# Kernel optimization log

Measured on AMD Instinct MI355X. Metric: run time of the kernel, lower is better.

The kernel has to match this reference:

```python
import jax, jax.numpy as jnp
import numpy as np

EPSILON = 0.1
N_ITERS = 5
SCALE = 0.05  # keeps exp(-cdist/epsilon) from underflowing to 0


def setup_inputs() -> dict:
    key = jax.random.key(0)
    k1, k2 = jax.random.split(key)
    P = jax.random.normal(k1, (8192, 64), dtype=jnp.float32) * SCALE
    Q = jax.random.normal(k2, (8192, 64), dtype=jnp.float32) * SCALE
    return {"P": P, "Q": Q}


def _cdist(P, Q):
    # Euclidean pairwise distances via the mm expansion (like torch.cdist p=2)
    sq = (jnp.sum(P * P, axis=-1)[:, None]
          + jnp.sum(Q * Q, axis=-1)[None, :]
          - 2.0 * P @ Q.T)
    return jnp.sqrt(jnp.maximum(sq, 0.0))


def reference(P, Q):
    C = _cdist(P, Q)                      # [N, N]
    K = jnp.exp(-C / EPSILON)             # [N, N]
    D = P.shape[1]
    u = jnp.ones((P.shape[0],), dtype=P.dtype) / D
    for _ in range(N_ITERS):              # small fixed iteration count
        v = 1.0 / (K @ u)                 # [N]
        u = 1.0 / (K @ v)                 # [N]
    plan = u[:, None] * K * v[None, :]    # [N, N]
    return jnp.sum(plan * C)
```

## Files before the change

kernel.cpp:

```cpp
#include <hip/hip_runtime.h>
#include <hip/hip_fp16.h>
#include <stdint.h>

#define NROWS 8192
#define DIM 64
#define EPS 0.1f

typedef float f32x4 __attribute__((ext_vector_type(4)));
typedef short s16x8 __attribute__((ext_vector_type(8)));
typedef _Float16 h2 __attribute__((ext_vector_type(2)));


__device__ __forceinline__ float wave_reduce_add(float v) {
  #pragma unroll
  for (int off = 32; off > 0; off >>= 1) v += __shfl_down(v, off, 64);
  return v;
}

__device__ __forceinline__ uint32_t pack_bf16_trunc(float x, float y) {
  return __builtin_amdgcn_perm(__float_as_uint(y), __float_as_uint(x), 0x07060302u);
}

__device__ __forceinline__ int pi_idx(int i) {
  int r = i & 63;
  int tj = r >> 4, quad = (r >> 2) & 3, e = r & 3;
  return (i & ~63) | (quad * 16 + tj * 4 + e);
}


#if __has_builtin(__builtin_amdgcn_cvt_scalef32_pk_f16_fp4)
#define CVT4H(kd, sel) __builtin_amdgcn_cvt_scalef32_pk_f16_fp4((kd), 1.0f, (sel))
#else
__device__ __forceinline__ h2 cvt4h_fb(uint32_t kd, int sel) {
  uint32_t byt  = (kd >> (sel * 8)) & 0xFFu;
  uint32_t selv = (byt & 0xFu) | ((byt >> 4) << 16);
  uint32_t tb = __builtin_amdgcn_perm(0x46444240u, 0x3E3C3800u, selv);
  uint32_t d  = ((tb & 0xFFu) << 8) | ((tb & 0xFF0000u) << 8);
  return __builtin_bit_cast(h2, d);
}
#define CVT4H(kd, sel) cvt4h_fb((kd), (sel))
#endif

#if __has_builtin(__builtin_amdgcn_cvt_scalef32_pk_fp4_f32)
__device__ __forceinline__ uint32_t enc4(float q0, float q1, float q2, float q3) {
  uint32_t pk = __builtin_amdgcn_cvt_scalef32_pk_fp4_f32(0u, q0, q1, 1.0f, 0);
  pk = __builtin_amdgcn_cvt_scalef32_pk_fp4_f32(pk, q2, q3, 1.0f, 1);
  return pk & 0xFFFFu;
}
#else
__device__ __forceinline__ uint32_t enc1(float q) {
  float c = fminf(floorf(2.f * q + 0.5f), 4.f);
  c += (q > 2.5f) ? 1.f : 0.f;
  c += (q > 3.5f) ? 1.f : 0.f;
  return (uint32_t)c;
}
__device__ __forceinline__ uint32_t enc4(float q0, float q1, float q2, float q3) {
  return enc1(q0) | (enc1(q1) << 4) | (enc1(q2) << 8) | (enc1(q3) << 12);
}
#endif

#if __has_builtin(__builtin_amdgcn_exp2f)
#define EXPD(d) __builtin_amdgcn_exp2f(-14.4269504089f * (d))
#else
#define EXPD(d) __expf(-10.0f * (d))
#endif

#define FP4DOT(kd, xv, acc)                                                          \
  acc = __builtin_amdgcn_fdot2(CVT4H((kd), 0), __builtin_bit_cast(h2, (xv).x), acc, false); \
  acc = __builtin_amdgcn_fdot2(CVT4H((kd), 1), __builtin_bit_cast(h2, (xv).y), acc, false); \
  acc = __builtin_amdgcn_fdot2(CVT4H((kd), 2), __builtin_bit_cast(h2, (xv).z), acc, false); \
  acc = __builtin_amdgcn_fdot2(CVT4H((kd), 3), __builtin_bit_cast(h2, (xv).w), acc, false);

#define FIN1(kd, xd_, sel)                                                           \
  {                                                                                  \
    uint32_t byt  = ((kd) >> ((sel) * 8)) & 0xFFu;                                   \
    uint32_t selv = (byt & 0xFu) | ((byt & 0xF0u) << 12);                            \
    uint32_t hi = __builtin_amdgcn_perm(0x4945423Du, 0x3800B500u, selv);             \
    uint32_t lo = __builtin_amdgcn_perm(0x608C978Cu, 0xDE008C00u, selv);             \
    h2 lut = __builtin_bit_cast(h2, lo | (hi << 8));                                 \
    h2 xp  = __builtin_bit_cast(h2, (xd_));                                          \
    s1b = __builtin_amdgcn_fdot2(CVT4H((kd), (sel)), xp, s1b, false);                \
    t2b = __builtin_amdgcn_fdot2(lut, xp, t2b, false);                               \
  }
#define FINDOT(kd, xv) FIN1(kd, (xv).x, 0) FIN1(kd, (xv).y, 1) FIN1(kd, (xv).z, 2) FIN1(kd, (xv).w, 3)


__global__ __launch_bounds__(256) void rownorm_pack(
    const float* __restrict__ P, const float* __restrict__ Q,
    float* __restrict__ p2, float* __restrict__ q2,
    unsigned short* __restrict__ Pb, unsigned short* __restrict__ Qb) {
  int g = blockIdx.x * 256 + threadIdx.x;
  int row = g >> 3, sub = g & 7;
  const float* X;
  float* out;
  unsigned short* Xb;
  int r;
  float sc;
  if (row < NROWS) { X = P; out = p2; Xb = Pb; r = row; sc = -2.f; }
  else             { X = Q; out = q2; Xb = Qb; r = row - NROWS; sc = 1.f; }
  const float4* X4 = (const float4*)(X + (size_t)r * DIM);
  float4 a0 = X4[sub * 2], a1 = X4[sub * 2 + 1];
  float ss = a0.x * a0.x + a0.y * a0.y + a0.z * a0.z + a0.w * a0.w
           + a1.x * a1.x + a1.y * a1.y + a1.z * a1.z + a1.w * a1.w;
  ss += __shfl_xor(ss, 1, 64);
  ss += __shfl_xor(ss, 2, 64);
  ss += __shfl_xor(ss, 4, 64);
  if (sub == 0) out[r] = ss;
  uint4 pk;
  pk.x = pack_bf16_trunc(sc * a0.x, sc * a0.y);
  pk.y = pack_bf16_trunc(sc * a0.z, sc * a0.w);
  pk.z = pack_bf16_trunc(sc * a1.x, sc * a1.y);
  pk.w = pack_bf16_trunc(sc * a1.z, sc * a1.w);
  *(uint4*)(Xb + (size_t)r * DIM + sub * 8) = pk;
}


struct KgenSmem {
  unsigned char A[128 * 128];
  unsigned char B[256 * 128];
};

__device__ __forceinline__ int swiz_off(int row, int kc) {
  return row * 128 + ((kc ^ (row & 7)) << 4);
}

__global__ __launch_bounds__(512) void kgen_kernel(
    const unsigned short* __restrict__ Pb, const unsigned short* __restrict__ Qb,
    const float* __restrict__ p2, const float* __restrict__ q2,
    unsigned char* __restrict__ K4, unsigned char* __restrict__ scales,
    float* __restrict__ rspart) {
  __shared__ KgenSmem sm;
  const int t  = threadIdx.x;
  const int bi = blockIdx.x * 128;
  const int bj = blockIdx.y * 256;

  {
    const uint4* Pb4 = (const uint4*)(Pb + (size_t)bi * DIM);
    const uint4* Qb4 = (const uint4*)(Qb + (size_t)bj * DIM);
    #pragma unroll
    for (int it = 0; it < 2; ++it) {
      int idx = t + it * 512;
      int row = idx >> 3, kc = idx & 7;
      *(uint4*)(sm.A + swiz_off(row, kc)) = Pb4[row * 8 + kc];
    }
    #pragma unroll
    for (int it = 0; it < 4; ++it) {
      int idx = t + it * 512;
      int row = idx >> 3, kc = idx & 7;
      *(uint4*)(sm.B + swiz_off(row, kc)) = Qb4[row * 8 + kc];
    }
  }
  __syncthreads();

  const int w        = t >> 6;
  const int lane     = t & 63;
  const int quad     = lane >> 4;
  const int m16      = lane & 15;
  const int wave_row = (w >> 2) * 64;
  const int wave_col = (w & 3) * 64;

  float pn[4];
  f32x4 qn[4];
  #pragma unroll
  for (int ti = 0; ti < 4; ++ti) pn[ti] = p2[bi + wave_row + ti * 16 + m16];
  #pragma unroll
  for (int tj = 0; tj < 4; ++tj)
    qn[tj] = *(const f32x4*)&q2[bj + wave_col + tj * 16 + quad * 4];

  f32x4 acc[4][4];
  #pragma unroll
  for (int ti = 0; ti < 4; ++ti)
    #pragma unroll
    for (int tj = 0; tj < 4; ++tj) acc[ti][tj] = qn[tj] + pn[ti];

  #pragma unroll
  for (int kstep = 0; kstep < 2; ++kstep) {
    const int kc = kstep * 4 + quad;
    s16x8 af[4], bf[4];
    #pragma unroll
    for (int ti = 0; ti < 4; ++ti)
      af[ti] = *(const s16x8*)(sm.A + swiz_off(wave_row + ti * 16 + m16, kc));
    #pragma unroll
    for (int tj = 0; tj < 4; ++tj)
      bf[tj] = *(const s16x8*)(sm.B + swiz_off(wave_col + tj * 16 + m16, kc));
    #pragma unroll
    for (int ti = 0; ti < 4; ++ti)
      #pragma unroll
      for (int tj = 0; tj < 4; ++tj)
        acc[ti][tj] = __builtin_amdgcn_mfma_f32_16x16x32_bf16(
            bf[tj], af[ti], acc[ti][tj], 0, 0, 0);
  }

  #pragma unroll
  for (int ti = 0; ti < 4; ++ti) {
    const int row = bi + wave_row + ti * 16 + m16;
    float kv[4][4];
    float mx = 0.f, rs = 0.f;
    #pragma unroll
    for (int tj = 0; tj < 4; ++tj) {
      f32x4 sq = acc[ti][tj];
      kv[tj][0] = EXPD(__builtin_amdgcn_sqrtf(fmaxf(sq.x, 0.f)));
      kv[tj][1] = EXPD(__builtin_amdgcn_sqrtf(fmaxf(sq.y, 0.f)));
      kv[tj][2] = EXPD(__builtin_amdgcn_sqrtf(fmaxf(sq.z, 0.f)));
      kv[tj][3] = EXPD(__builtin_amdgcn_sqrtf(fmaxf(sq.w, 0.f)));
      float mt = fmaxf(fmaxf(kv[tj][0], kv[tj][1]), fmaxf(kv[tj][2], kv[tj][3]));
      mx = fmaxf(mx, mt);
      rs += (kv[tj][0] + kv[tj][1]) + (kv[tj][2] + kv[tj][3]);
    }
    mx = fmaxf(mx, __shfl_xor(mx, 16, 64));
    uint32_t eb = (__float_as_uint(mx) >> 23) - 1u;
    float si = __uint_as_float((254u - eb) << 23);
    uint32_t pk0 = enc4(kv[0][0] * si, kv[0][1] * si, kv[0][2] * si, kv[0][3] * si);
    uint32_t pk1 = enc4(kv[1][0] * si, kv[1][1] * si, kv[1][2] * si, kv[1][3] * si);
    uint32_t pk2 = enc4(kv[2][0] * si, kv[2][1] * si, kv[2][2] * si, kv[2][3] * si);
    uint32_t pk3 = enc4(kv[3][0] * si, kv[3][1] * si, kv[3][2] * si, kv[3][3] * si);
    uint2 st = uint2{pk0 | (pk1 << 16), pk2 | (pk3 << 16)};
    *(uint2*)(K4 + (size_t)row * (NROWS / 2) + ((bj + wave_col) >> 1) + quad * 8) = st;
    uint32_t eb2 = (uint32_t)__shfl_xor((int)eb, 32, 64);
    if (quad == 0) {
      *(unsigned short*)(scales + (size_t)row * 256 + ((bj + wave_col) >> 5)) =
          (unsigned short)((eb & 0xFFu) | ((eb2 & 0xFFu) << 8));
    }
    float v = rs;
    v += __shfl_xor(v, 16, 64);
    v += __shfl_xor(v, 32, 64);
    if (quad == 0)
      rspart[(size_t)(blockIdx.y * 4 + (w & 3)) * NROWS + row] = v;
  }
}

__global__ __launch_bounds__(128) void v1_kernel(const float* __restrict__ rspart,
                                                 unsigned short* __restrict__ vb16) {
  int i = blockIdx.x * 128 + threadIdx.x;
  float s = 0.f;
  #pragma unroll 8
  for (int c = 0; c < 128; ++c) s += rspart[(size_t)c * NROWS + i];
  vb16[pi_idx(i)] = __half_as_ushort(__float2half(64.0f / s));
}


__global__ __launch_bounds__(256) void matvec_fp4(
    const unsigned char* __restrict__ K4, const unsigned char* __restrict__ scales,
    const unsigned short* __restrict__ xin, unsigned short* __restrict__ yout) {
  const int t = threadIdx.x, lane = t & 63, w = t >> 6;
  const int bk = blockIdx.x & 7, j = blockIdx.x >> 3;
  const int panel = ((j >> 3) << 3) | bk;
  const int r0 = panel * 128 + (j & 7) * 16 + w * 4;
  const uint4* kr0 = (const uint4*)(K4 + (size_t)r0 * (NROWS / 2));
  const uint4* kr1 = (const uint4*)(K4 + (size_t)(r0 + 1) * (NROWS / 2));
  const uint4* kr2 = (const uint4*)(K4 + (size_t)(r0 + 2) * (NROWS / 2));
  const uint4* kr3 = (const uint4*)(K4 + (size_t)(r0 + 3) * (NROWS / 2));
  const unsigned char* sr0 = scales + (size_t)r0 * 256;
  const unsigned char* sr1 = sr0 + 256;
  const unsigned char* sr2 = sr0 + 512;
  const unsigned char* sr3 = sr0 + 768;
  const uint4* x4 = (const uint4*)xin;

  int b = lane;
  uint4 nx0 = x4[b * 4 + 0], nx1 = x4[b * 4 + 1];
  uint4 nx2 = x4[b * 4 + 2], nx3 = x4[b * 4 + 3];
  uint4 nk0 = kr0[b], nk1 = kr1[b], nk2 = kr2[b], nk3 = kr3[b];

  float t0 = 0.f, t1 = 0.f, t2 = 0.f, t3 = 0.f;
  #pragma unroll
  for (int s = 0; s < 4; ++s) {
    uint4 cx0 = nx0, cx1 = nx1, cx2 = nx2, cx3 = nx3;
    uint4 ck0 = nk0, ck1 = nk1, ck2 = nk2, ck3 = nk3;
    uint32_t sb0 = sr0[b], sb1 = sr1[b], sb2 = sr2[b], sb3 = sr3[b];
    if (s < 3) {
      int bn = b + 64;
      nx0 = x4[bn * 4 + 0]; nx1 = x4[bn * 4 + 1];
      nx2 = x4[bn * 4 + 2]; nx3 = x4[bn * 4 + 3];
      nk0 = kr0[bn]; nk1 = kr1[bn]; nk2 = kr2[bn]; nk3 = kr3[bn];
      b = bn;
    }
    float a0, a1;
    a0 = 0.f; a1 = 0.f;
    FP4DOT(ck0.x, cx0, a0) FP4DOT(ck0.y, cx1, a1)
    FP4DOT(ck0.z, cx2, a0) FP4DOT(ck0.w, cx3, a1)
    t0 = fmaf(__uint_as_float(sb0 << 23), a0 + a1, t0);
    a0 = 0.f; a1 = 0.f;
    FP4DOT(ck1.x, cx0, a0) FP4DOT(ck1.y, cx1, a1)
    FP4DOT(ck1.z, cx2, a0) FP4DOT(ck1.w, cx3, a1)
    t1 = fmaf(__uint_as_float(sb1 << 23), a0 + a1, t1);
    a0 = 0.f; a1 = 0.f;
    FP4DOT(ck2.x, cx0, a0) FP4DOT(ck2.y, cx1, a1)
    FP4DOT(ck2.z, cx2, a0) FP4DOT(ck2.w, cx3, a1)
    t2 = fmaf(__uint_as_float(sb2 << 23), a0 + a1, t2);
    a0 = 0.f; a1 = 0.f;
    FP4DOT(ck3.x, cx0, a0) FP4DOT(ck3.y, cx1, a1)
    FP4DOT(ck3.z, cx2, a0) FP4DOT(ck3.w, cx3, a1)
    t3 = fmaf(__uint_as_float(sb3 << 23), a0 + a1, t3);
  }

  t0 = wave_reduce_add(t0);
  t1 = wave_reduce_add(t1);
  t2 = wave_reduce_add(t2);
  t3 = wave_reduce_add(t3);
  if (lane == 0) {
    yout[pi_idx(r0 + 0)] = __half_as_ushort(__float2half(1.0f / t0));
    yout[pi_idx(r0 + 1)] = __half_as_ushort(__float2half(1.0f / t1));
    yout[pi_idx(r0 + 2)] = __half_as_ushort(__float2half(1.0f / t2));
    yout[pi_idx(r0 + 3)] = __half_as_ushort(__float2half(1.0f / t3));
  }
}


__global__ __launch_bounds__(256) void final_fp4(
    const unsigned char* __restrict__ K4, const unsigned char* __restrict__ scales,
    const unsigned short* __restrict__ xin, float* __restrict__ partials) {
  const int t = threadIdx.x, lane = t & 63, w = t >> 6;
  const int p = w >> 1, h = w & 1;
  const int bk = blockIdx.x & 7, j = blockIdx.x >> 3;
  const int panel = ((j >> 5) << 3) | bk;
  const int r0 = panel * 128 + (j & 31) * 4 + p * 2;
  const uint4* krow0 = (const uint4*)(K4 + (size_t)r0 * (NROWS / 2));
  const uint4* krow1 = (const uint4*)(K4 + (size_t)(r0 + 1) * (NROWS / 2));
  const unsigned char* srow0 = scales + (size_t)r0 * 256;
  const unsigned char* srow1 = srow0 + 256;
  const uint4* x4 = (const uint4*)xin;
  const int b0 = h * 128 + lane;
  const int b1 = b0 + 64;

  uint4 xa0 = x4[b0 * 4 + 0], xb0 = x4[b0 * 4 + 1];
  uint4 xc0 = x4[b0 * 4 + 2], xd0 = x4[b0 * 4 + 3];
  uint4 xa1 = x4[b1 * 4 + 0], xb1 = x4[b1 * 4 + 1];
  uint4 xc1 = x4[b1 * 4 + 2], xd1 = x4[b1 * 4 + 3];
  uint4 k00 = krow0[b0], k01 = krow0[b1];
  uint4 k10 = krow1[b0], k11 = krow1[b1];
  uint32_t sb00 = srow0[b0], sb01 = srow0[b1];
  uint32_t sb10 = srow1[b0], sb11 = srow1[b1];

  float s1_0, s2_0, s1_1, s2_1;
  {
    float S = __uint_as_float(sb00 << 23);
    float lnS = ((float)(int)sb00 - 127.f) * 0.69314718f;
    float s1b = 0.f, t2b = 0.f;
    FINDOT(k00.x, xa0) FINDOT(k00.y, xb0) FINDOT(k00.z, xc0) FINDOT(k00.w, xd0)
    s1_0 = S * s1b;
    s2_0 = S * fmaf(lnS, s1b, t2b);
  }
  {
    float S = __uint_as_float(sb01 << 23);
    float lnS = ((float)(int)sb01 - 127.f) * 0.69314718f;
    float s1b = 0.f, t2b = 0.f;
    FINDOT(k01.x, xa1) FINDOT(k01.y, xb1) FINDOT(k01.z, xc1) FINDOT(k01.w, xd1)
    s1_0 = fmaf(S, s1b, s1_0);
    s2_0 = fmaf(S, fmaf(lnS, s1b, t2b), s2_0);
  }
  {
    float S = __uint_as_float(sb10 << 23);
    float lnS = ((float)(int)sb10 - 127.f) * 0.69314718f;
    float s1b = 0.f, t2b = 0.f;
    FINDOT(k10.x, xa0) FINDOT(k10.y, xb0) FINDOT(k10.z, xc0) FINDOT(k10.w, xd0)
    s1_1 = S * s1b;
    s2_1 = S * fmaf(lnS, s1b, t2b);
  }
  {
    float S = __uint_as_float(sb11 << 23);
    float lnS = ((float)(int)sb11 - 127.f) * 0.69314718f;
    float s1b = 0.f, t2b = 0.f;
    FINDOT(k11.x, xa1) FINDOT(k11.y, xb1) FINDOT(k11.z, xc1) FINDOT(k11.w, xd1)
    s1_1 = fmaf(S, s1b, s1_1);
    s2_1 = fmaf(S, fmaf(lnS, s1b, t2b), s2_1);
  }

  s1_0 = wave_reduce_add(s1_0);
  s2_0 = wave_reduce_add(s2_0);
  s1_1 = wave_reduce_add(s1_1);
  s2_1 = wave_reduce_add(s2_1);
  __shared__ float sred[4][4];
  if (lane == 0) {
    sred[w][0] = s1_0; sred[w][1] = s2_0; sred[w][2] = s1_1; sred[w][3] = s2_1;
  }
  __syncthreads();
  if (t == 0) {
    float acc = 0.f;
    #pragma unroll
    for (int pp = 0; pp < 2; ++pp)
      #pragma unroll
      for (int jj = 0; jj < 2; ++jj) {
        float s1 = sred[pp * 2 + 0][jj * 2 + 0] + sred[pp * 2 + 1][jj * 2 + 0];
        float s2 = sred[pp * 2 + 0][jj * 2 + 1] + sred[pp * 2 + 1][jj * 2 + 1];
        acc += s2 / s1;
      }
    partials[blockIdx.x] = (-EPS) * acc;
  }
}

__global__ __launch_bounds__(256) void reduce_kernel(
    const float* __restrict__ partials, float* __restrict__ out) {
  const int t = threadIdx.x;
  float s = 0.f;
  #pragma unroll
  for (int i = 0; i < 8; ++i) s += partials[t + i * 256];
  s = wave_reduce_add(s);
  __shared__ float red[4];
  int lane = t & 63, wid = t >> 6;
  if (lane == 0) red[wid] = s;
  __syncthreads();
  if (t == 0) out[0] = red[0] + red[1] + red[2] + red[3];
}


extern "C" void kernel_launch(void* const* d_in, const int* in_sizes, int n_in,
                              void* d_out, int out_size, void* d_ws, size_t ws_size,
                              hipStream_t stream) {
  const float* P = (const float*)d_in[0];
  const float* Q = (const float*)d_in[1];
  float* out = (float*)d_out;

  char* ws = (char*)d_ws;
  unsigned char* K4     = (unsigned char*)ws;
  unsigned char* scales = (unsigned char*)(ws + 33554432);
  float* rspart   = (float*)(ws + 35651584);
  float* p2       = (float*)(ws + 39845888);
  float* q2       = (float*)(ws + 39878656);
  float* partials = (float*)(ws + 39911424);
  unsigned short* ub16 = (unsigned short*)(ws + 39919616);
  unsigned short* vb16 = ub16 + NROWS;
  unsigned short* Pb   = (unsigned short*)(ws + 39952384);
  unsigned short* Qb   = (unsigned short*)(ws + 41000960);

  rownorm_pack<<<512, 256, 0, stream>>>(P, Q, p2, q2, Pb, Qb);
  kgen_kernel<<<dim3(NROWS / 128, NROWS / 256), 512, 0, stream>>>(
      Pb, Qb, p2, q2, K4, scales, rspart);
  v1_kernel<<<NROWS / 128, 128, 0, stream>>>(rspart, vb16);

  for (int m = 1; m < 9; ++m) {
    const unsigned short* xin = (m & 1) ? vb16 : ub16;
    unsigned short* yout      = (m & 1) ? ub16 : vb16;
    matvec_fp4<<<NROWS / 16, 256, 0, stream>>>(K4, scales, xin, yout);
  }

  final_fp4<<<NROWS / 4, 256, 0, stream>>>(K4, scales, vb16, partials);
  reduce_kernel<<<1, 256, 0, stream>>>(partials, out);
}
```

Baseline: 173.9 us.

## Pre-tile bf16 operands in MFMA fragment order and load directly from global

```diff
diff --git a/kernel.cpp b/kernel.cpp
--- a/kernel.cpp
+++ b/kernel.cpp
@@ -88,12 +88,12 @@
 __global__ __launch_bounds__(256) void rownorm_pack(
     const float* __restrict__ P, const float* __restrict__ Q,
     float* __restrict__ p2, float* __restrict__ q2,
-    unsigned short* __restrict__ Pb, unsigned short* __restrict__ Qb) {
+    uint4* __restrict__ Pb, uint4* __restrict__ Qb) {
   int g = blockIdx.x * 256 + threadIdx.x;
   int row = g >> 3, sub = g & 7;
   const float* X;
   float* out;
-  unsigned short* Xb;
+  uint4* Xb;
   int r;
   float sc;
   if (row < NROWS) { X = P; out = p2; Xb = Pb; r = row; sc = -2.f; }
@@ -111,46 +111,18 @@
   pk.y = pack_bf16_trunc(sc * a0.z, sc * a0.w);
   pk.z = pack_bf16_trunc(sc * a1.x, sc * a1.y);
   pk.w = pack_bf16_trunc(sc * a1.z, sc * a1.w);
-  *(uint4*)(Xb + (size_t)r * DIM + sub * 8) = pk;
-}
-
-
-struct KgenSmem {
-  unsigned char A[128 * 128];
-  unsigned char B[256 * 128];
-};
-
-__device__ __forceinline__ int swiz_off(int row, int kc) {
-  return row * 128 + ((kc ^ (row & 7)) << 4);
-}
+  Xb[(((r >> 4) * 8 + sub) << 4) + (r & 15)] = pk;
+}
+
 
 __global__ __launch_bounds__(512) void kgen_kernel(
-    const unsigned short* __restrict__ Pb, const unsigned short* __restrict__ Qb,
+    const uint4* __restrict__ Pb, const uint4* __restrict__ Qb,
     const float* __restrict__ p2, const float* __restrict__ q2,
     unsigned char* __restrict__ K4, unsigned char* __restrict__ scales,
     float* __restrict__ rspart) {
-  __shared__ KgenSmem sm;
   const int t  = threadIdx.x;
   const int bi = blockIdx.x * 128;
   const int bj = blockIdx.y * 256;
-
-  {
-    const uint4* Pb4 = (const uint4*)(Pb + (size_t)bi * DIM);
-    const uint4* Qb4 = (const uint4*)(Qb + (size_t)bj * DIM);
-    #pragma unroll
-    for (int it = 0; it < 2; ++it) {
-      int idx = t + it * 512;
-      int row = idx >> 3, kc = idx & 7;
-      *(uint4*)(sm.A + swiz_off(row, kc)) = Pb4[row * 8 + kc];
-    }
-    #pragma unroll
-    for (int it = 0; it < 4; ++it) {
-      int idx = t + it * 512;
-      int row = idx >> 3, kc = idx & 7;
-      *(uint4*)(sm.B + swiz_off(row, kc)) = Qb4[row * 8 + kc];
-    }
-  }
-  __syncthreads();
 
   const int w        = t >> 6;
   const int lane     = t & 63;
@@ -159,6 +131,11 @@
   const int wave_row = (w >> 2) * 64;
   const int wave_col = (w & 3) * 64;
 
+  const s16x8* Pw = (const s16x8*)Pb;
+  const s16x8* Qw = (const s16x8*)Qb;
+  const int gp = (bi + wave_row) >> 4;
+  const int gq = (bj + wave_col) >> 4;
+
   float pn[4];
   f32x4 qn[4];
   #pragma unroll
@@ -179,10 +156,10 @@
     s16x8 af[4], bf[4];
     #pragma unroll
     for (int ti = 0; ti < 4; ++ti)
-      af[ti] = *(const s16x8*)(sm.A + swiz_off(wave_row + ti * 16 + m16, kc));
+      af[ti] = Pw[((gp + ti) * 8 + kc) * 16 + m16];
     #pragma unroll
     for (int tj = 0; tj < 4; ++tj)
-      bf[tj] = *(const s16x8*)(sm.B + swiz_off(wave_col + tj * 16 + m16, kc));
+      bf[tj] = Qw[((gq + tj) * 8 + kc) * 16 + m16];
     #pragma unroll
     for (int ti = 0; ti < 4; ++ti)
       #pragma unroll
@@ -419,8 +396,8 @@
   float* partials = (float*)(ws + 39911424);
   unsigned short* ub16 = (unsigned short*)(ws + 39919616);
   unsigned short* vb16 = ub16 + NROWS;
-  unsigned short* Pb   = (unsigned short*)(ws + 39952384);
-  unsigned short* Qb   = (unsigned short*)(ws + 41000960);
+  uint4* Pb = (uint4*)(ws + 39952384);
+  uint4* Qb = (uint4*)(ws + 41000960);
 
   rownorm_pack<<<512, 256, 0, stream>>>(P, Q, p2, q2, Pb, Qb);
   kgen_kernel<<<dim3(NROWS / 128, NROWS / 256), 512, 0, stream>>>(
```

New measurement: 170.9 us (median of 2 runs). About the same (-1.7%).
